# Kernel tuning notes

Hardware: AMD Instinct MI355X
Metric: run time of the kernel (lower is better)

Reference implementation:

```python
import jax, jax.numpy as jnp
import numpy as np

BN_EPS = 1e-5


def setup_inputs() -> dict:
    key = jax.random.key(0)
    ks = jax.random.split(key, 10)
    B, C2, Hh, Ww = 4, 64, 64, 64  # in_channels=128, C/2=64
    C = 2 * C2
    inp = {
        "H": jax.random.normal(ks[0], (B, C2, Hh, Ww), jnp.float32),
        "L": jax.random.normal(ks[1], (B, C2, Hh, Ww), jnp.float32),
        # 1x1 convs stored as [out, in] matrices
        "theta_w": jax.random.normal(ks[2], (C2, C), jnp.float32) * (1.0 / np.sqrt(C)),
        "theta_b": jnp.zeros((C2,), jnp.float32),
        "phi_w": jax.random.normal(ks[3], (C2, C), jnp.float32) * (1.0 / np.sqrt(C)),
        "phi_b": jnp.zeros((C2,), jnp.float32),
        "g_w": jax.random.normal(ks[4], (C2, C2), jnp.float32) * (1.0 / np.sqrt(C2)),
        "g_b": jnp.zeros((C2,), jnp.float32),
        # 3x3 conv of CBR block, OIHW
        "conv_w": jax.random.normal(ks[5], (C2, C2, 3, 3), jnp.float32) * (1.0 / np.sqrt(C2 * 9)),
        "conv_b": jnp.zeros((C2,), jnp.float32),
        # BatchNorm (inference-mode) params
        "bn_gamma": jnp.ones((C2,), jnp.float32),
        "bn_beta": jnp.zeros((C2,), jnp.float32),
        "bn_mean": jnp.zeros((C2,), jnp.float32),
        "bn_var": jnp.ones((C2,), jnp.float32),
    }
    return inp


def reference(H, L, theta_w, theta_b, phi_w, phi_b, g_w, g_b,
              conv_w, conv_b, bn_gamma, bn_beta, bn_mean, bn_var):
    B, C2, h, w = L.shape
    N = h * w
    HL = jnp.concatenate([H, L], axis=1)  # [B, C, h, w]
    # 1x1 conv projections as channel matmuls
    A = jnp.einsum('oc,bchw->bohw', theta_w, HL) + theta_b[:, None, None]  # [B,C2,h,w]
    Bm = jnp.einsum('oc,bchw->bohw', phi_w, HL) + phi_b[:, None, None]
    A = A.reshape(B, C2, N).transpose(0, 2, 1)   # [B, N, C2]
    Bm = Bm.reshape(B, C2, N)                    # [B, C2, N]
    M = jnp.einsum('bnc,bcm->bnm', A, Bm)        # [B, N, N], unscaled
    M = jax.nn.softmax(M, axis=1)                # softmax over FIRST spatial axis (dim=1)
    D = jnp.einsum('oc,bchw->bohw', g_w, L) + g_b[:, None, None]
    D = D.reshape(B, C2, N)                      # [B, C2, N]
    E = jnp.einsum('bcn,bnm->bcm', D, M)         # [B, C2, N]
    E = E.reshape(B, C2, h, w)
    # CBR: conv3x3(pad=1) -> BatchNorm (inference) -> ReLU
    F = jax.lax.conv_general_dilated(
        E, conv_w, window_strides=(1, 1), padding='SAME',
        dimension_numbers=('NCHW', 'OIHW', 'NCHW')) + conv_b[None, :, None, None]
    F = (F - bn_mean[None, :, None, None]) * jax.lax.rsqrt(bn_var + BN_EPS)[None, :, None, None]
    F = F * bn_gamma[None, :, None, None] + bn_beta[None, :, None, None]
    F = jax.nn.relu(F)
    return H + F
```

## Files before the change

kernel.cpp:

```cpp
#include <hip/hip_runtime.h>

typedef __bf16 bf16;
typedef unsigned short u16;
typedef __attribute__((ext_vector_type(8))) __bf16 bf16x8;
typedef __attribute__((ext_vector_type(16))) float f32x16;
typedef __attribute__((ext_vector_type(2))) unsigned int uint2v;
typedef __attribute__((ext_vector_type(4))) unsigned int uint4v;

#define MFMA32(a, b, c) __builtin_amdgcn_mfma_f32_32x32x16_bf16(a, b, c, 0, 0, 0)

__device__ __forceinline__ u16 bbits(float f) {
  bf16 h = (bf16)f;
  return __builtin_bit_cast(u16, h);
}
__device__ __forceinline__ float bf2f(u16 u) {
  return (float)__builtin_bit_cast(bf16, u);
}
__device__ __forceinline__ bf16x8 ldg16(const u16* p) {
  return *reinterpret_cast<const bf16x8*>(p);
}
__device__ __forceinline__ bf16x8 ld_p8(const u16* p) {
  uint2v a = *reinterpret_cast<const uint2v*>(p);
  uint2v b = *reinterpret_cast<const uint2v*>(p + 4);
  uint4v u;
  u.x = a.x; u.y = a.y; u.z = b.x; u.w = b.y;
  return __builtin_bit_cast(bf16x8, u);
}
__device__ __forceinline__ unsigned packbf(float a, float b) {
  return (unsigned)bbits(a) | ((unsigned)bbits(b) << 16);
}
__device__ __forceinline__ void split8(const float* xv, bf16x8& hi, bf16x8& lo) {
  uint4v hv, lv;
#pragma unroll
  for (int jp = 0; jp < 4; ++jp) {
    float a0 = xv[2 * jp], a1 = xv[2 * jp + 1];
    u16 h0 = bbits(a0), h1 = bbits(a1);
    u16 l0 = bbits(a0 - bf2f(h0)), l1 = bbits(a1 - bf2f(h1));
    unsigned hh = (unsigned)h0 | ((unsigned)h1 << 16);
    unsigned ll = (unsigned)l0 | ((unsigned)l1 << 16);
    if (jp == 0) { hv.x = hh; lv.x = ll; }
    else if (jp == 1) { hv.y = hh; lv.y = ll; }
    else if (jp == 2) { hv.z = hh; lv.z = ll; }
    else { hv.w = hh; lv.w = ll; }
  }
  hi = __builtin_bit_cast(bf16x8, hv);
  lo = __builtin_bit_cast(bf16x8, lv);
}


__global__ __launch_bounds__(256) void pa_prep(
    const float* __restrict__ cw, const float* __restrict__ cbias,
    const float* __restrict__ gamma, const float* __restrict__ beta,
    const float* __restrict__ mean, const float* __restrict__ var,
    const float* __restrict__ tw, const float* __restrict__ pw, const float* __restrict__ gw,
    u16* __restrict__ Wt, float* __restrict__ bnA, float* __restrict__ bnB,
    u16* __restrict__ Wth, u16* __restrict__ Wtl,
    u16* __restrict__ Wph, u16* __restrict__ Wpl,
    u16* __restrict__ Wgh, u16* __restrict__ Wgl) {
  int i = blockIdx.x * 256 + threadIdx.x;
  if (i < 36864) {
    int ci = i & 63, co = (i >> 6) & 63, s = i >> 12;
    int kc = ci >> 4, q2c = (ci >> 3) & 1, j = ci & 7;
    int lane = q2c * 32 + (co & 31);
    int cbi = co >> 5;
    Wt[(((s * 4 + kc) * 2 + cbi) * 64 + lane) * 8 + j] = bbits(cw[(co * 64 + ci) * 9 + s]);
  }
  if (i < 16384) {
    int ii = i & 8191;
    int j = ii & 7, l = (ii >> 3) & 63, f = ii >> 9;
    int out = (f & 1) * 32 + (l & 31);
    int in = (f >> 1) * 16 + (l >> 5) * 8 + j;
    const float* W = (i < 8192) ? tw : pw;
    float v = W[out * 128 + in];
    u16 h = bbits(v);
    u16 lo = bbits(v - bf2f(h));
    if (i < 8192) { Wth[ii] = h; Wtl[ii] = lo; }
    else { Wph[ii] = h; Wpl[ii] = lo; }
  } else if (i < 20480) {
    int ii = i - 16384;
    int j = ii & 7, l = (ii >> 3) & 63, f = ii >> 9;
    int out = (f & 1) * 32 + (l & 31);
    int in = (f >> 1) * 16 + (l >> 5) * 8 + j;
    float v = gw[out * 64 + in];
    u16 h = bbits(v);
    Wgh[ii] = h;
    Wgl[ii] = bbits(v - bf2f(h));
  }
  if (i < 64) {
    float rs = rsqrtf(var[i] + 1e-5f);
    float A = gamma[i] * rs;
    bnA[i] = A;
    bnB[i] = (cbias[i] - mean[i]) * A + beta[i];
  }
}

template <bool LO>
__device__ __forceinline__ void store_qk_swz(const f32x16& a0, const f32x16& a1,
                                             const float* __restrict__ bias,
                                             u16* __restrict__ Hi, u16* __restrict__ Lo,
                                             int base, int l31, int q2) {
#pragma unroll
  for (int mt = 0; mt < 2; ++mt) {
    const f32x16& A = mt ? a1 : a0;
#pragma unroll
    for (int rq = 0; rq < 4; ++rq) {
      int ch = mt * 32 + rq * 8 + q2 * 4;
      float4 bb = *reinterpret_cast<const float4*>(bias + ch);
      float v0 = A[rq * 4 + 0] + bb.x;
      float v1 = A[rq * 4 + 1] + bb.y;
      float v2 = A[rq * 4 + 2] + bb.z;
      float v3 = A[rq * 4 + 3] + bb.w;
      int off = base + ((mt * 2 + (rq >> 1)) * 64 + l31 + 32 * (rq & 1)) * 8 + q2 * 4;
      u16 h0 = bbits(v0), h1 = bbits(v1), h2 = bbits(v2), h3 = bbits(v3);
      uint2v hv;
      hv.x = (unsigned)h0 | ((unsigned)h1 << 16);
      hv.y = (unsigned)h2 | ((unsigned)h3 << 16);
      *reinterpret_cast<uint2v*>(Hi + off) = hv;
      if (LO) {
        u16 l0 = bbits(v0 - bf2f(h0)), l1 = bbits(v1 - bf2f(h1));
        u16 l2 = bbits(v2 - bf2f(h2)), l3 = bbits(v3 - bf2f(h3));
        uint2v lv;
        lv.x = (unsigned)l0 | ((unsigned)l1 << 16);
        lv.y = (unsigned)l2 | ((unsigned)l3 << 16);
        *reinterpret_cast<uint2v*>(Lo + off) = lv;
      }
    }
  }
}

template <int NS>
__device__ __forceinline__ void gemm3(const u16* __restrict__ Wh, const u16* __restrict__ Wl,
                                      const bf16x8* Bh, const bf16x8* Bl,
                                      int lane, f32x16& a0, f32x16& a1) {
#pragma unroll
  for (int s = 0; s < NS; ++s) {
    bf16x8 w0h = ldg16(Wh + ((s * 2 + 0) * 64 + lane) * 8);
    bf16x8 w0l = ldg16(Wl + ((s * 2 + 0) * 64 + lane) * 8);
    bf16x8 w1h = ldg16(Wh + ((s * 2 + 1) * 64 + lane) * 8);
    bf16x8 w1l = ldg16(Wl + ((s * 2 + 1) * 64 + lane) * 8);
    a0 = MFMA32(w0h, Bh[s], a0);
    a0 = MFMA32(w0h, Bl[s], a0);
    a0 = MFMA32(w0l, Bh[s], a0);
    a1 = MFMA32(w1h, Bh[s], a1);
    a1 = MFMA32(w1h, Bl[s], a1);
    a1 = MFMA32(w1l, Bh[s], a1);
  }
}

template <int NS>
__device__ __forceinline__ void gemm2(const u16* __restrict__ Wh,
                                      const bf16x8* Bh, const bf16x8* Bl,
                                      int lane, f32x16& a0, f32x16& a1) {
#pragma unroll
  for (int s = 0; s < NS; ++s) {
    bf16x8 w0h = ldg16(Wh + ((s * 2 + 0) * 64 + lane) * 8);
    bf16x8 w1h = ldg16(Wh + ((s * 2 + 1) * 64 + lane) * 8);
    a0 = MFMA32(w0h, Bh[s], a0);
    a0 = MFMA32(w0h, Bl[s], a0);
    a1 = MFMA32(w1h, Bh[s], a1);
    a1 = MFMA32(w1h, Bl[s], a1);
  }
}

__global__ __launch_bounds__(384, 2) void pa_proj(
    const float* __restrict__ H, const float* __restrict__ L,
    const float* __restrict__ tb, const float* __restrict__ pb, const float* __restrict__ gb,
    const u16* __restrict__ Wth, const u16* __restrict__ Wph, const u16* __restrict__ Wpl,
    const u16* __restrict__ Wgh,
    u16* __restrict__ Qh, u16* __restrict__ Ql,
    u16* __restrict__ Kh, u16* __restrict__ V) {
  int b = blockIdx.x >> 6;
  int tile64 = blockIdx.x & 63;
  int w = threadIdx.x >> 6;
  int lane = threadIdx.x & 63;
  int l31 = lane & 31, q2 = lane >> 5;
  int half = w & 1, role = w >> 1;
  int tile32 = tile64 * 2 + half;
  int n = tile32 * 32 + l31;
  int base = tile32 * 2048;

  if (role < 2) {
    bf16x8 Bh[8], Bl[8];
#pragma unroll
    for (int s = 0; s < 8; ++s) {
      const float* src = (s < 4) ? (H + (b * 64 + s * 16) * 4096)
                                 : (L + (b * 64 + (s - 4) * 16) * 4096);
      const float* pp = src + (q2 * 8) * 4096 + n;
      float xv[8];
#pragma unroll
      for (int j = 0; j < 8; ++j) xv[j] = pp[j * 4096];
      split8(xv, Bh[s], Bl[s]);
    }
    f32x16 a0 = {}, a1 = {};
    if (role == 0) {
      gemm2<8>(Wth, Bh, Bl, lane, a0, a1);
      store_qk_swz<false>(a0, a1, tb, Kh + b * 262144, (u16*)nullptr, base, l31, q2);
    } else {
      gemm3<8>(Wph, Wpl, Bh, Bl, lane, a0, a1);
      store_qk_swz<true>(a0, a1, pb, Qh + b * 262144, Ql + b * 262144, base, l31, q2);
    }
  } else {
    bf16x8 Bh[4], Bl[4];
#pragma unroll
    for (int s = 0; s < 4; ++s) {
      const float* pp = L + (b * 64 + s * 16 + q2 * 8) * 4096 + n;
      float xv[8];
#pragma unroll
      for (int j = 0; j < 8; ++j) xv[j] = pp[j * 4096];
      split8(xv, Bh[s], Bl[s]);
    }
    f32x16 a0 = {}, a1 = {};
    gemm2<4>(Wgh, Bh, Bl, lane, a0, a1);
    u16* Vb = V + b * 262144;
    int kch = (l31 >> 4) & 1, q2v = (l31 >> 3) & 1, jn = l31 & 7;
#pragma unroll
    for (int mt = 0; mt < 2; ++mt) {
      const f32x16& A = mt ? a1 : a0;
#pragma unroll
      for (int rq = 0; rq < 4; ++rq) {
        int ch = mt * 32 + rq * 8 + q2 * 4;
        float4 bb = *reinterpret_cast<const float4*>(gb + ch);
        float vv[4] = {A[rq * 4 + 0] + bb.x, A[rq * 4 + 1] + bb.y,
                       A[rq * 4 + 2] + bb.z, A[rq * 4 + 3] + bb.w};
#pragma unroll
        for (int i2 = 0; i2 < 4; ++i2) {
          int c31 = rq * 8 + q2 * 4 + i2;
          int lane_v = c31 + 32 * q2v;
          Vb[(((tile32 * 2 + kch) * 2 + mt) * 64 + lane_v) * 8 + jn] = bbits(vv[i2]);
        }
      }
    }
  }
}

__global__ __launch_bounds__(512, 4) void pa_flash(
    const u16* __restrict__ Qhg, const u16* __restrict__ Qlg,
    const u16* __restrict__ Khg, const u16* __restrict__ Vg, u16* __restrict__ E) {
  __shared__ float Obuf[64 * 33];
  __shared__ float MLm[8 * 32];
  __shared__ float MLl[8 * 32];
  __shared__ float Lst[32];

  int tid = threadIdx.x;
  int w = tid >> 6, lane = tid & 63;
  int l31 = lane & 31, q2 = lane >> 5;
  int b = blockIdx.x >> 7, mt = blockIdx.x & 127;
  int m0 = mt * 32;
  int bq = b * 4096;
  const u16* Qb = Qhg + b * 262144;
  const u16* Qlb = Qlg + b * 262144;
  const u16* Kb = Khg + b * 262144;
  const u16* Vb = Vg + b * 262144;

  bf16x8 qh[4], ql[4];
#pragma unroll
  for (int kc = 0; kc < 4; ++kc) {
    qh[kc] = ldg16(Qb + ((mt * 4 + kc) * 64 + lane) * 8);
    ql[kc] = ldg16(Qlb + ((mt * 4 + kc) * 64 + lane) * 8);
  }

  f32x16 accO[2] = {};
  float Mm = 0.f, Ll = 0.f;

  bf16x8 kh[4];
#pragma unroll
  for (int kc = 0; kc < 4; ++kc) kh[kc] = ldg16(Kb + ((w * 4 + kc) * 64 + lane) * 8);

#pragma unroll 1
  for (int it = 0; it < 16; ++it) {
    int tile = it * 8 + w;

    bf16x8 vf[2][2];
#pragma unroll
    for (int kch = 0; kch < 2; ++kch)
#pragma unroll
      for (int cbi = 0; cbi < 2; ++cbi)
        vf[cbi][kch] = ldg16(Vb + (((tile * 2 + kch) * 2 + cbi) * 64 + lane) * 8);

    f32x16 a = {};
#pragma unroll
    for (int kc = 0; kc < 4; ++kc) {
      a = MFMA32(kh[kc], qh[kc], a);
      a = MFMA32(kh[kc], ql[kc], a);
    }
    int tn = (it < 15) ? tile + 8 : tile;
#pragma unroll
    for (int kc = 0; kc < 4; ++kc) kh[kc] = ldg16(Kb + ((tn * 4 + kc) * 64 + lane) * 8);

    if (it == 0) {
      float tmax = a[0];
#pragma unroll
      for (int r = 1; r < 16; ++r) tmax = fmaxf(tmax, a[r]);
      tmax = fmaxf(tmax, __shfl_xor(tmax, 32, 64));
      Mm = tmax;
    }
    float pv[16];
    float psum = 0.f;
#pragma unroll
    for (int r = 0; r < 16; ++r) {
      pv[r] = __expf(a[r] - Mm);
      psum += pv[r];
    }
    psum += __shfl_xor(psum, 32, 64);
    Ll += psum;

    unsigned pd[4][2];
#pragma unroll
    for (int q = 0; q < 4; ++q) {
      pd[q][0] = packbf(pv[q * 4 + 0], pv[q * 4 + 1]);
      pd[q][1] = packbf(pv[q * 4 + 2], pv[q * 4 + 3]);
    }
    unsigned xd[4][2];
#pragma unroll
    for (int q = 0; q < 4; ++q) {
      xd[q][0] = (unsigned)__shfl_xor((int)pd[q][0], 32, 64);
      xd[q][1] = (unsigned)__shfl_xor((int)pd[q][1], 32, 64);
    }
    uint4v u0, u1;
    u0.x = q2 ? xd[1][0] : pd[0][0];
    u0.y = q2 ? xd[1][1] : pd[0][1];
    u0.z = q2 ? pd[1][0] : xd[0][0];
    u0.w = q2 ? pd[1][1] : xd[0][1];
    u1.x = q2 ? xd[3][0] : pd[2][0];
    u1.y = q2 ? xd[3][1] : pd[2][1];
    u1.z = q2 ? pd[3][0] : xd[2][0];
    u1.w = q2 ? pd[3][1] : xd[2][1];
    bf16x8 p0 = __builtin_bit_cast(bf16x8, u0);
    bf16x8 p1 = __builtin_bit_cast(bf16x8, u1);

    accO[0] = MFMA32(vf[0][0], p0, accO[0]);
    accO[0] = MFMA32(vf[0][1], p1, accO[0]);
    accO[1] = MFMA32(vf[1][0], p0, accO[1]);
    accO[1] = MFMA32(vf[1][1], p1, accO[1]);
  }

  if (q2 == 0) {
    MLm[w * 32 + l31] = Mm;
    MLl[w * 32 + l31] = Ll;
  }
  __syncthreads();
  float M = MLm[l31];
  for (int ww = 1; ww < 8; ++ww) M = fmaxf(M, MLm[ww * 32 + l31]);
  float ls = 0.f;
  for (int ww = 0; ww < 8; ++ww) ls += MLl[ww * 32 + l31] * __expf(MLm[ww * 32 + l31] - M);
  float mysc = __expf(Mm - M);
  if (w == 0 && q2 == 0) Lst[l31] = ls;
  for (int ww = 0; ww < 8; ++ww) {
    if (w == ww) {
#pragma unroll
      for (int cbi = 0; cbi < 2; ++cbi)
#pragma unroll
        for (int r = 0; r < 16; ++r) {
          int c = cbi * 32 + (r & 3) + 8 * (r >> 2) + 4 * q2;
          float* dst = &Obuf[c * 33 + l31];
          float v = accO[cbi][r] * mysc;
          if (ww == 0)
            *dst = v;
          else
            *dst += v;
        }
    }
    __syncthreads();
  }
  int em = tid >> 4, ec0 = (tid & 15) * 4;
  float invl = 1.0f / Lst[em];
  float v0 = Obuf[(ec0 + 0) * 33 + em] * invl;
  float v1 = Obuf[(ec0 + 1) * 33 + em] * invl;
  float v2 = Obuf[(ec0 + 2) * 33 + em] * invl;
  float v3 = Obuf[(ec0 + 3) * 33 + em] * invl;
  uint2v u0;
  u0.x = packbf(v0, v1);
  u0.y = packbf(v2, v3);
  *reinterpret_cast<uint2v*>(E + (bq + m0 + em) * 64 + ec0) = u0;
}

__global__ __launch_bounds__(512) void pa_conv(
    const u16* __restrict__ E, const u16* __restrict__ Wt,
    const float* __restrict__ bnA, const float* __restrict__ bnB,
    const float* __restrict__ H, float* __restrict__ out) {
  __shared__ u16 Er[3][66 * 68];
  __shared__ float Rbuf[4][64 * 17];
  int tid = threadIdx.x;
  int blk = blockIdx.x;
  int b = blk >> 6, y = blk & 63;
  int lane = tid & 63;
  int l31 = lane & 31, q2 = lane >> 5;
  int wv = tid >> 6;
  int ks = wv & 1, mb = (wv >> 1) & 1, cbi = wv >> 2;
  int s0 = (y == 0) ? 1 : 0;
  int s1 = (y == 63) ? 1 : 2;

  for (int s = s0; s <= s1; ++s) {
    int yy = y + s - 1;
    int x = tid >> 3, co = (tid & 7) * 8;
    const uint2v* src = reinterpret_cast<const uint2v*>(E + ((b * 4096 + yy * 64 + x) * 64 + co));
    uint2v a = src[0], b4 = src[1];
    u16* d = &Er[s][(x + 1) * 68 + co];
    *reinterpret_cast<uint2v*>(d) = a;
    *reinterpret_cast<uint2v*>(d + 4) = b4;
  }
  if (tid < 96) {
    int s = tid >> 5, side = (tid >> 4) & 1, co = (tid & 15) * 4;
    uint2v z;
    z.x = 0;
    z.y = 0;
    *reinterpret_cast<uint2v*>(&Er[s][(side ? 65 : 0) * 68 + co]) = z;
  }
  __syncthreads();

  f32x16 a0 = {}, a1 = {};
  for (int s = s0; s <= s1; ++s) {
#pragma unroll
    for (int dx = 0; dx < 3; ++dx) {
      int s3 = s * 3 + dx;
      int kcA = ks * 2, kcB = ks * 2 + 1;
      bf16x8 wa = ldg16(Wt + (((s3 * 4 + kcA) * 2 + cbi) * 64 + lane) * 8);
      bf16x8 wb = ldg16(Wt + (((s3 * 4 + kcB) * 2 + cbi) * 64 + lane) * 8);
      bf16x8 ea = ld_p8(&Er[s][(mb * 32 + l31 + dx) * 68 + kcA * 16 + q2 * 8]);
      bf16x8 eb = ld_p8(&Er[s][(mb * 32 + l31 + dx) * 68 + kcB * 16 + q2 * 8]);
      a0 = MFMA32(wa, ea, a0);
      a1 = MFMA32(wb, eb, a1);
    }
  }
  int p = cbi * 2 + mb;
  if (ks == 1) {
#pragma unroll
    for (int r = 0; r < 16; ++r) Rbuf[p][lane * 17 + r] = a0[r] + a1[r];
  }
  __syncthreads();
  if (ks == 0) {
#pragma unroll
    for (int r = 0; r < 16; ++r) {
      int c = cbi * 32 + (r & 3) + 8 * (r >> 2) + 4 * q2;
      int x = mb * 32 + l31;
      float v = a0[r] + a1[r] + Rbuf[p][lane * 17 + r];
      v = v * bnA[c] + bnB[c];
      v = fmaxf(v, 0.f);
      int idx = ((b * 64 + c) * 64 + y) * 64 + x;
      out[idx] = H[idx] + v;
    }
  }
}

extern "C" void kernel_launch(void* const* d_in, const int* in_sizes, int n_in,
                              void* d_out, int out_size, void* d_ws, size_t ws_size,
                              hipStream_t stream) {
  (void)in_sizes; (void)n_in; (void)out_size; (void)ws_size;
  const float* H = (const float*)d_in[0];
  const float* L = (const float*)d_in[1];
  const float* tw = (const float*)d_in[2];
  const float* tb = (const float*)d_in[3];
  const float* pw = (const float*)d_in[4];
  const float* pb = (const float*)d_in[5];
  const float* gw = (const float*)d_in[6];
  const float* gb = (const float*)d_in[7];
  const float* cw = (const float*)d_in[8];
  const float* cb = (const float*)d_in[9];
  const float* gamma = (const float*)d_in[10];
  const float* beta = (const float*)d_in[11];
  const float* mean = (const float*)d_in[12];
  const float* var = (const float*)d_in[13];

  const int NC = 16384 * 64;
  u16* Qh = (u16*)d_ws;
  u16* Ql = Qh + NC;
  u16* Kh = Ql + NC;
  u16* Vv = Kh + NC;
  u16* Eb = Vv + NC;
  u16* Wt = Eb + NC;
  float* bnA = (float*)(Wt + 36864);
  float* bnB = bnA + 64;
  u16* Wth = (u16*)(bnB + 64);
  u16* Wtl = Wth + 8192;
  u16* Wph = Wtl + 8192;
  u16* Wpl = Wph + 8192;
  u16* Wgh = Wpl + 8192;
  u16* Wgl = Wgh + 4096;

  pa_prep<<<144, 256, 0, stream>>>(cw, cb, gamma, beta, mean, var, tw, pw, gw,
                                   Wt, bnA, bnB, Wth, Wtl, Wph, Wpl, Wgh, Wgl);
  pa_proj<<<256, 384, 0, stream>>>(H, L, tb, pb, gb, Wth, Wph, Wpl, Wgh,
                                   Qh, Ql, Kh, Vv);
  pa_flash<<<512, 512, 0, stream>>>(Qh, Ql, Kh, Vv, Eb);
  pa_conv<<<256, 512, 0, stream>>>(Eb, Wt, bnA, bnB, H, (float*)d_out);
}
```

Baseline: 135.5 us.

## Double flash query tile per block and split projection K across wave pairs

```diff
diff --git a/kernel.cpp b/kernel.cpp
--- a/kernel.cpp
+++ b/kernel.cpp
@@ -162,57 +162,77 @@
   }
 }
 
-__global__ __launch_bounds__(384, 2) void pa_proj(
+__global__ __launch_bounds__(384, 3) void pa_proj(
     const float* __restrict__ H, const float* __restrict__ L,
     const float* __restrict__ tb, const float* __restrict__ pb, const float* __restrict__ gb,
     const u16* __restrict__ Wth, const u16* __restrict__ Wph, const u16* __restrict__ Wpl,
     const u16* __restrict__ Wgh,
     u16* __restrict__ Qh, u16* __restrict__ Ql,
     u16* __restrict__ Kh, u16* __restrict__ V) {
-  int b = blockIdx.x >> 6;
-  int tile64 = blockIdx.x & 63;
+  __shared__ float Rb[3 * 64 * 33];
+  int b = blockIdx.x >> 7;
+  int t = blockIdx.x & 127;
   int w = threadIdx.x >> 6;
   int lane = threadIdx.x & 63;
   int l31 = lane & 31, q2 = lane >> 5;
-  int half = w & 1, role = w >> 1;
-  int tile32 = tile64 * 2 + half;
-  int n = tile32 * 32 + l31;
-  int base = tile32 * 2048;
-
+  int role = w >> 1, kh2 = w & 1;
+  int n = t * 32 + l31;
+  int base = t * 2048;
+
+  f32x16 a0 = {}, a1 = {};
   if (role < 2) {
-    bf16x8 Bh[8], Bl[8];
-#pragma unroll
-    for (int s = 0; s < 8; ++s) {
+    bf16x8 Bh[4], Bl[4];
+#pragma unroll
+    for (int si = 0; si < 4; ++si) {
+      int s = kh2 * 4 + si;
       const float* src = (s < 4) ? (H + (b * 64 + s * 16) * 4096)
                                  : (L + (b * 64 + (s - 4) * 16) * 4096);
       const float* pp = src + (q2 * 8) * 4096 + n;
       float xv[8];
 #pragma unroll
       for (int j = 0; j < 8; ++j) xv[j] = pp[j * 4096];
-      split8(xv, Bh[s], Bl[s]);
-    }
-    f32x16 a0 = {}, a1 = {};
-    if (role == 0) {
-      gemm2<8>(Wth, Bh, Bl, lane, a0, a1);
-      store_qk_swz<false>(a0, a1, tb, Kh + b * 262144, (u16*)nullptr, base, l31, q2);
-    } else {
-      gemm3<8>(Wph, Wpl, Bh, Bl, lane, a0, a1);
-      store_qk_swz<true>(a0, a1, pb, Qh + b * 262144, Ql + b * 262144, base, l31, q2);
-    }
+      split8(xv, Bh[si], Bl[si]);
+    }
+    if (role == 0)
+      gemm2<4>(Wth + kh2 * 4096, Bh, Bl, lane, a0, a1);
+    else
+      gemm3<4>(Wph + kh2 * 4096, Wpl + kh2 * 4096, Bh, Bl, lane, a0, a1);
   } else {
-    bf16x8 Bh[4], Bl[4];
-#pragma unroll
-    for (int s = 0; s < 4; ++s) {
+    bf16x8 Bh[2], Bl[2];
+#pragma unroll
+    for (int si = 0; si < 2; ++si) {
+      int s = kh2 * 2 + si;
       const float* pp = L + (b * 64 + s * 16 + q2 * 8) * 4096 + n;
       float xv[8];
 #pragma unroll
       for (int j = 0; j < 8; ++j) xv[j] = pp[j * 4096];
-      split8(xv, Bh[s], Bl[s]);
-    }
-    f32x16 a0 = {}, a1 = {};
-    gemm2<4>(Wgh, Bh, Bl, lane, a0, a1);
+      split8(xv, Bh[si], Bl[si]);
+    }
+    gemm2<2>(Wgh + kh2 * 2048, Bh, Bl, lane, a0, a1);
+  }
+
+  float* rp = Rb + (role * 64 + lane) * 33;
+  if (kh2 == 1) {
+#pragma unroll
+    for (int r = 0; r < 16; ++r) rp[r] = a0[r];
+#pragma unroll
+    for (int r = 0; r < 16; ++r) rp[16 + r] = a1[r];
+  }
+  __syncthreads();
+  if (kh2 == 1) return;
+#pragma unroll
+  for (int r = 0; r < 16; ++r) a0[r] += rp[r];
+#pragma unroll
+  for (int r = 0; r < 16; ++r) a1[r] += rp[16 + r];
+
+  if (role == 0) {
+    store_qk_swz<false>(a0, a1, tb, Kh + b * 262144, (u16*)nullptr, base, l31, q2);
+  } else if (role == 1) {
+    store_qk_swz<true>(a0, a1, pb, Qh + b * 262144, Ql + b * 262144, base, l31, q2);
+  } else {
     u16* Vb = V + b * 262144;
     int kch = (l31 >> 4) & 1, q2v = (l31 >> 3) & 1, jn = l31 & 7;
+    (void)kch; (void)q2v; (void)jn;
 #pragma unroll
     for (int mt = 0; mt < 2; ++mt) {
       const f32x16& A = mt ? a1 : a0;
@@ -225,42 +245,48 @@
 #pragma unroll
         for (int i2 = 0; i2 < 4; ++i2) {
           int c31 = rq * 8 + q2 * 4 + i2;
-          int lane_v = c31 + 32 * q2v;
-          Vb[(((tile32 * 2 + kch) * 2 + mt) * 64 + lane_v) * 8 + jn] = bbits(vv[i2]);
+          int kch2 = (l31 >> 4) & 1, q2v2 = (l31 >> 3) & 1, jn2 = l31 & 7;
+          int lane_v = c31 + 32 * q2v2;
+          Vb[(((t * 2 + kch2) * 2 + mt) * 64 + lane_v) * 8 + jn2] = bbits(vv[i2]);
         }
       }
     }
   }
 }
 
-__global__ __launch_bounds__(512, 4) void pa_flash(
+__global__ __launch_bounds__(512, 2) void pa_flash(
     const u16* __restrict__ Qhg, const u16* __restrict__ Qlg,
     const u16* __restrict__ Khg, const u16* __restrict__ Vg, u16* __restrict__ E) {
-  __shared__ float Obuf[64 * 33];
-  __shared__ float MLm[8 * 32];
-  __shared__ float MLl[8 * 32];
-  __shared__ float Lst[32];
+  __shared__ float Obuf[64 * 67];
+  __shared__ float MLm[8 * 2 * 32];
+  __shared__ float MLl[8 * 2 * 32];
+  __shared__ float Lst[64];
 
   int tid = threadIdx.x;
   int w = tid >> 6, lane = tid & 63;
   int l31 = lane & 31, q2 = lane >> 5;
-  int b = blockIdx.x >> 7, mt = blockIdx.x & 127;
-  int m0 = mt * 32;
+  int blk = blockIdx.x;
+  int xcd = blk & 7;
+  int b = xcd >> 1;
+  int mt = ((blk >> 3) << 1) | (xcd & 1);
+  int m0 = mt * 64;
   int bq = b * 4096;
   const u16* Qb = Qhg + b * 262144;
   const u16* Qlb = Qlg + b * 262144;
   const u16* Kb = Khg + b * 262144;
   const u16* Vb = Vg + b * 262144;
 
-  bf16x8 qh[4], ql[4];
-#pragma unroll
-  for (int kc = 0; kc < 4; ++kc) {
-    qh[kc] = ldg16(Qb + ((mt * 4 + kc) * 64 + lane) * 8);
-    ql[kc] = ldg16(Qlb + ((mt * 4 + kc) * 64 + lane) * 8);
-  }
-
-  f32x16 accO[2] = {};
-  float Mm = 0.f, Ll = 0.f;
+  bf16x8 qh[2][4], ql[2][4];
+#pragma unroll
+  for (int mb = 0; mb < 2; ++mb)
+#pragma unroll
+    for (int kc = 0; kc < 4; ++kc) {
+      qh[mb][kc] = ldg16(Qb + (((mt * 2 + mb) * 4 + kc) * 64 + lane) * 8);
+      ql[mb][kc] = ldg16(Qlb + (((mt * 2 + mb) * 4 + kc) * 64 + lane) * 8);
+    }
+
+  f32x16 accO[2][2] = {};
+  float Mm[2] = {0.f, 0.f}, Ll[2] = {0.f, 0.f};
 
   bf16x8 kh[4];
 #pragma unroll
@@ -277,101 +303,123 @@
       for (int cbi = 0; cbi < 2; ++cbi)
         vf[cbi][kch] = ldg16(Vb + (((tile * 2 + kch) * 2 + cbi) * 64 + lane) * 8);
 
-    f32x16 a = {};
-#pragma unroll
-    for (int kc = 0; kc < 4; ++kc) {
-      a = MFMA32(kh[kc], qh[kc], a);
-      a = MFMA32(kh[kc], ql[kc], a);
+    f32x16 s[2];
+#pragma unroll
+    for (int mb = 0; mb < 2; ++mb) {
+      f32x16 a = {};
+#pragma unroll
+      for (int kc = 0; kc < 4; ++kc) {
+        a = MFMA32(kh[kc], qh[mb][kc], a);
+        a = MFMA32(kh[kc], ql[mb][kc], a);
+      }
+      s[mb] = a;
     }
     int tn = (it < 15) ? tile + 8 : tile;
 #pragma unroll
     for (int kc = 0; kc < 4; ++kc) kh[kc] = ldg16(Kb + ((tn * 4 + kc) * 64 + lane) * 8);
 
-    if (it == 0) {
-      float tmax = a[0];
-#pragma unroll
-      for (int r = 1; r < 16; ++r) tmax = fmaxf(tmax, a[r]);
-      tmax = fmaxf(tmax, __shfl_xor(tmax, 32, 64));
-      Mm = tmax;
-    }
-    float pv[16];
-    float psum = 0.f;
-#pragma unroll
-    for (int r = 0; r < 16; ++r) {
-      pv[r] = __expf(a[r] - Mm);
-      psum += pv[r];
-    }
-    psum += __shfl_xor(psum, 32, 64);
-    Ll += psum;
-
-    unsigned pd[4][2];
-#pragma unroll
-    for (int q = 0; q < 4; ++q) {
-      pd[q][0] = packbf(pv[q * 4 + 0], pv[q * 4 + 1]);
-      pd[q][1] = packbf(pv[q * 4 + 2], pv[q * 4 + 3]);
-    }
-    unsigned xd[4][2];
-#pragma unroll
-    for (int q = 0; q < 4; ++q) {
-      xd[q][0] = (unsigned)__shfl_xor((int)pd[q][0], 32, 64);
-      xd[q][1] = (unsigned)__shfl_xor((int)pd[q][1], 32, 64);
-    }
-    uint4v u0, u1;
-    u0.x = q2 ? xd[1][0] : pd[0][0];
-    u0.y = q2 ? xd[1][1] : pd[0][1];
-    u0.z = q2 ? pd[1][0] : xd[0][0];
-    u0.w = q2 ? pd[1][1] : xd[0][1];
-    u1.x = q2 ? xd[3][0] : pd[2][0];
-    u1.y = q2 ? xd[3][1] : pd[2][1];
-    u1.z = q2 ? pd[3][0] : xd[2][0];
-    u1.w = q2 ? pd[3][1] : xd[2][1];
-    bf16x8 p0 = __builtin_bit_cast(bf16x8, u0);
-    bf16x8 p1 = __builtin_bit_cast(bf16x8, u1);
-
-    accO[0] = MFMA32(vf[0][0], p0, accO[0]);
-    accO[0] = MFMA32(vf[0][1], p1, accO[0]);
-    accO[1] = MFMA32(vf[1][0], p0, accO[1]);
-    accO[1] = MFMA32(vf[1][1], p1, accO[1]);
+#pragma unroll
+    for (int mb = 0; mb < 2; ++mb) {
+      if (it == 0) {
+        float tmax = s[mb][0];
+#pragma unroll
+        for (int r = 1; r < 16; ++r) tmax = fmaxf(tmax, s[mb][r]);
+        tmax = fmaxf(tmax, __shfl_xor(tmax, 32, 64));
+        Mm[mb] = tmax;
+      }
+      float pv[16];
+      float psum = 0.f;
+#pragma unroll
+      for (int r = 0; r < 16; ++r) {
+        pv[r] = __expf(s[mb][r] - Mm[mb]);
+        psum += pv[r];
+      }
+      psum += __shfl_xor(psum, 32, 64);
+      Ll[mb] += psum;
+
+      unsigned pd[4][2];
+#pragma unroll
+      for (int q = 0; q < 4; ++q) {
+        pd[q][0] = packbf(pv[q * 4 + 0], pv[q * 4 + 1]);
+        pd[q][1] = packbf(pv[q * 4 + 2], pv[q * 4 + 3]);
+      }
+      unsigned xd[4][2];
+#pragma unroll
+      for (int q = 0; q < 4; ++q) {
+        xd[q][0] = (unsigned)__shfl_xor((int)pd[q][0], 32, 64);
+        xd[q][1] = (unsigned)__shfl_xor((int)pd[q][1], 32, 64);
+      }
+      uint4v u0, u1;
+      u0.x = q2 ? xd[1][0] : pd[0][0];
+      u0.y = q2 ? xd[1][1] : pd[0][1];
+      u0.z = q2 ? pd[1][0] : xd[0][0];
+      u0.w = q2 ? pd[1][1] : xd[0][1];
+      u1.x = q2 ? xd[3][0] : pd[2][0];
+      u1.y = q2 ? xd[3][1] : pd[2][1];
+      u1.z = q2 ? pd[3][0] : xd[2][0];
+      u1.w = q2 ? pd[3][1] : xd[2][1];
+      bf16x8 p0 = __builtin_bit_cast(bf16x8, u0);
+      bf16x8 p1 = __builtin_bit_cast(bf16x8, u1);
+
+      accO[0][mb] = MFMA32(vf[0][0], p0, accO[0][mb]);
+      accO[0][mb] = MFMA32(vf[0][1], p1, accO[0][mb]);
+      accO[1][mb] = MFMA32(vf[1][0], p0, accO[1][mb]);
+      accO[1][mb] = MFMA32(vf[1][1], p1, accO[1][mb]);
+    }
   }
 
   if (q2 == 0) {
-    MLm[w * 32 + l31] = Mm;
-    MLl[w * 32 + l31] = Ll;
+#pragma unroll
+    for (int mb = 0; mb < 2; ++mb) {
+      MLm[(w * 2 + mb) * 32 + l31] = Mm[mb];
+      MLl[(w * 2 + mb) * 32 + l31] = Ll[mb];
+    }
   }
   __syncthreads();
-  float M = MLm[l31];
-  for (int ww = 1; ww < 8; ++ww) M = fmaxf(M, MLm[ww * 32 + l31]);
-  float ls = 0.f;
-  for (int ww = 0; ww < 8; ++ww) ls += MLl[ww * 32 + l31] * __expf(MLm[ww * 32 + l31] - M);
-  float mysc = __expf(Mm - M);
-  if (w == 0 && q2 == 0) Lst[l31] = ls;
+  float mysc[2];
+#pragma unroll
+  for (int mb = 0; mb < 2; ++mb) {
+    float M = MLm[mb * 32 + l31];
+    for (int ww = 1; ww < 8; ++ww) M = fmaxf(M, MLm[(ww * 2 + mb) * 32 + l31]);
+    float ls = 0.f;
+    for (int ww = 0; ww < 8; ++ww)
+      ls += MLl[(ww * 2 + mb) * 32 + l31] * __expf(MLm[(ww * 2 + mb) * 32 + l31] - M);
+    mysc[mb] = __expf(Mm[mb] - M);
+    if (w == 0 && q2 == 0) Lst[mb * 32 + l31] = ls;
+  }
   for (int ww = 0; ww < 8; ++ww) {
     if (w == ww) {
 #pragma unroll
       for (int cbi = 0; cbi < 2; ++cbi)
 #pragma unroll
-        for (int r = 0; r < 16; ++r) {
-          int c = cbi * 32 + (r & 3) + 8 * (r >> 2) + 4 * q2;
-          float* dst = &Obuf[c * 33 + l31];
-          float v = accO[cbi][r] * mysc;
-          if (ww == 0)
-            *dst = v;
-          else
-            *dst += v;
+        for (int mb = 0; mb < 2; ++mb) {
+          float sc = mysc[mb];
+#pragma unroll
+          for (int r = 0; r < 16; ++r) {
+            int c = cbi * 32 + (r & 3) + 8 * (r >> 2) + 4 * q2;
+            int m = mb * 32 + l31;
+            float* dst = &Obuf[c * 67 + m];
+            float v = accO[cbi][mb][r] * sc;
+            if (ww == 0)
+              *dst = v;
+            else
+              *dst += v;
+          }
         }
     }
     __syncthreads();
   }
-  int em = tid >> 4, ec0 = (tid & 15) * 4;
+  int em = tid >> 3, ec0 = (tid & 7) * 8;
   float invl = 1.0f / Lst[em];
-  float v0 = Obuf[(ec0 + 0) * 33 + em] * invl;
-  float v1 = Obuf[(ec0 + 1) * 33 + em] * invl;
-  float v2 = Obuf[(ec0 + 2) * 33 + em] * invl;
-  float v3 = Obuf[(ec0 + 3) * 33 + em] * invl;
-  uint2v u0;
-  u0.x = packbf(v0, v1);
-  u0.y = packbf(v2, v3);
-  *reinterpret_cast<uint2v*>(E + (bq + m0 + em) * 64 + ec0) = u0;
+  float vals[8];
+#pragma unroll
+  for (int j = 0; j < 8; ++j) vals[j] = Obuf[(ec0 + j) * 67 + em] * invl;
+  uint4v u0;
+  u0.x = packbf(vals[0], vals[1]);
+  u0.y = packbf(vals[2], vals[3]);
+  u0.z = packbf(vals[4], vals[5]);
+  u0.w = packbf(vals[6], vals[7]);
+  *reinterpret_cast<uint4v*>(E + (bq + m0 + em) * 64 + ec0) = u0;
 }
 
 __global__ __launch_bounds__(512) void pa_conv(
@@ -479,8 +527,8 @@
 
   pa_prep<<<144, 256, 0, stream>>>(cw, cb, gamma, beta, mean, var, tw, pw, gw,
                                    Wt, bnA, bnB, Wth, Wtl, Wph, Wpl, Wgh, Wgl);
-  pa_proj<<<256, 384, 0, stream>>>(H, L, tb, pb, gb, Wth, Wph, Wpl, Wgh,
+  pa_proj<<<512, 384, 0, stream>>>(H, L, tb, pb, gb, Wth, Wph, Wpl, Wgh,
                                    Qh, Ql, Kh, Vv);
-  pa_flash<<<512, 512, 0, stream>>>(Qh, Ql, Kh, Vv, Eb);
+  pa_flash<<<256, 512, 0, stream>>>(Qh, Ql, Kh, Vv, Eb);
   pa_conv<<<256, 512, 0, stream>>>(Eb, Wt, bnA, bnB, H, (float*)d_out);
 }
```

Result: no change. 136.1 us (+0.5%).
